# Optimization experiments

Hardware: AMD Instinct MI355X
Metric: run time of the kernel (lower is better)

Reference implementation:

```python
import jax, jax.numpy as jnp
import numpy as np

EMB_DIM = 1024
HEAD_DIM = 128
BLOCK_SIZE = 2048
BATCH = 8


def setup_inputs() -> dict:
    key = jax.random.key(0)
    kx, kq, kk, kv = jax.random.split(key, 4)
    x = jax.random.normal(kx, (BATCH, BLOCK_SIZE, EMB_DIM), dtype=jnp.float32)
    # nn.Linear(emb_dim, head_dim, bias=False) weights have shape [head_dim, emb_dim]
    s = 1.0 / np.sqrt(EMB_DIM)
    Wq = jax.random.uniform(kq, (HEAD_DIM, EMB_DIM), jnp.float32, -s, s)
    Wk = jax.random.uniform(kk, (HEAD_DIM, EMB_DIM), jnp.float32, -s, s)
    Wv = jax.random.uniform(kv, (HEAD_DIM, EMB_DIM), jnp.float32, -s, s)
    return {"x": x, "Wq": Wq, "Wk": Wk, "Wv": Wv}


def reference(x, Wq, Wk, Wv):
    # x: [b, t, c]; W*: [h, c]  (torch Linear applies x @ W.T)
    b, t, c = x.shape
    h = Wq.shape[0]
    q = jnp.einsum("btc,hc->bth", x, Wq)
    k = jnp.einsum("btc,hc->bth", x, Wk)
    v = jnp.einsum("btc,hc->bth", x, Wv)
    scores = jnp.einsum("bth,bsh->bts", q, k) * (h ** -0.5)  # [b, t, t]
    causal = jnp.tril(jnp.ones((t, t), dtype=bool))
    scores = jnp.where(causal, scores, -jnp.inf)
    attn = jax.nn.softmax(scores, axis=-1)
    # dropout is identity in eval / deterministic mode
    return jnp.einsum("bts,bsh->bth", attn, v)
```

## Files before the change

### kernel.cpp

```cpp
#include <hip/hip_runtime.h>
#include <hip/hip_bf16.h>

#define TT 2048
#define CC 1024
#define DD 128
#define BB 8
#define BK 32
#define NSTEP (CC / BK)

typedef __attribute__((ext_vector_type(8))) short bf16x8;
typedef __attribute__((ext_vector_type(4))) float f32x4;
typedef __attribute__((ext_vector_type(16))) float f32x16;
typedef __attribute__((ext_vector_type(4))) short short4v;

__device__ inline short f2bf(float f) {
    union { float f; unsigned u; } v; v.f = f;
    unsigned r = v.u + 0x7FFFu + ((v.u >> 16) & 1u);
    return (short)(r >> 16);
}

__device__ inline unsigned pack2(float lo, float hi) {
    return (unsigned)(unsigned short)f2bf(lo) | ((unsigned)(unsigned short)f2bf(hi) << 16);
}

#define GLOAD16(gp, lp) __builtin_amdgcn_global_load_lds(                       \
    (const __attribute__((address_space(1))) unsigned int*)(const void*)(gp),   \
    (__attribute__((address_space(3))) unsigned int*)(void*)(lp), 16, 0, 0)

__global__ __launch_bounds__(256) void prep_w(const float* __restrict__ Wq,
                                              const float* __restrict__ Wk,
                                              const float* __restrict__ Wv,
                                              short* __restrict__ Wall) {
    int row = blockIdx.x;
    const float* src = row < 128 ? Wq + (size_t)row * CC
                     : row < 256 ? Wk + (size_t)(row - 128) * CC
                                 : Wv + (size_t)(row - 256) * CC;
    short* dst = Wall + (size_t)row * CC;
    int j = threadIdx.x * 4;
    float4 f = *(const float4*)(src + j);
    short4v s = { f2bf(f.x), f2bf(f.y), f2bf(f.z), f2bf(f.w) };
    *(short4v*)(dst + j) = s;
}

__global__ __launch_bounds__(256) void qkv_fused(const float* __restrict__ X,
                                                 const short* __restrict__ Wall,
                                                 short* __restrict__ Q,
                                                 short* __restrict__ K,
                                                 short* __restrict__ Vs) {
    __shared__ char lds[2 * 16384];
    int tid = threadIdx.x, lane = tid & 63, wid = tid >> 6;
    int wm = wid >> 1, wn = wid & 1;
    int lg = lane >> 4, lr = lane & 15;
    int m0 = blockIdx.x * 64;
    int n0 = blockIdx.y * 128;

    int rA = tid >> 3;
    int cA = (tid & 7) * 16;
    int sA = cA ^ ((rA & 7) << 4);
    const char* gA0 = (const char*)(X + (size_t)(m0 + rA) * CC) + sA;
    const char* gA1 = (const char*)(X + (size_t)(m0 + rA + 32) * CC) + sA;
    int rB = tid >> 2, cB = (tid & 3) * 16;
    const char* gB0 = (const char*)(Wall + (size_t)(n0 + rB) * CC) + cB;
    const char* gB1 = (const char*)(Wall + (size_t)(n0 + rB + 64) * CC) + cB;

    f32x4 acc[2][4] = {};

#define STAGEF(t_, buf_) do {                                                   \
        char* b_ = lds + (buf_) * 16384;                                        \
        size_t ka_ = (size_t)(t_) * 128;             \
        size_t kb_ = (size_t)(t_) * 64;              \
        GLOAD16(gA0 + ka_, b_ + tid * 16);                                      \
        GLOAD16(gA1 + ka_, b_ + 4096 + tid * 16);                               \
        GLOAD16(gB0 + kb_, b_ + 8192 + tid * 16);                               \
        GLOAD16(gB1 + kb_, b_ + 12288 + tid * 16);                              \
    } while (0)

#define KSTEPF(buf_) do {                                                       \
        const char* b_ = lds + (buf_) * 16384;                                  \
        bf16x8 a_[2], bb_[4];                                                   \
        int swz_ = (lr & 7) << 4;                                               \
        _Pragma("unroll")                                                       \
        for (int mi = 0; mi < 2; ++mi) {                                        \
            const char* Ap_ = b_ + (wm * 32 + mi * 16 + lr) * 128;              \
            f32x4 lo_ = *(const f32x4*)(Ap_ + ((lg * 32) ^ swz_));              \
            f32x4 hi_ = *(const f32x4*)(Ap_ + ((lg * 32 + 16) ^ swz_));         \
            bf16x8 t_;                                                          \
            t_[0] = f2bf(lo_[0]); t_[1] = f2bf(lo_[1]);                         \
            t_[2] = f2bf(lo_[2]); t_[3] = f2bf(lo_[3]);                         \
            t_[4] = f2bf(hi_[0]); t_[5] = f2bf(hi_[1]);                         \
            t_[6] = f2bf(hi_[2]); t_[7] = f2bf(hi_[3]);                         \
            a_[mi] = t_;                                                        \
        }                                                                       \
        _Pragma("unroll")                                                       \
        for (int nj = 0; nj < 4; ++nj)                                          \
            bb_[nj] = *(const bf16x8*)(b_ + 8192 + (wn*64 + nj*16 + lr) * 64 + lg*16);\
        _Pragma("unroll")                                                       \
        for (int mi = 0; mi < 2; ++mi)                                          \
            _Pragma("unroll")                                                   \
            for (int nj = 0; nj < 4; ++nj)                                      \
                acc[mi][nj] = __builtin_amdgcn_mfma_f32_16x16x32_bf16(a_[mi], bb_[nj], acc[mi][nj], 0, 0, 0);\
    } while (0)

    STAGEF(0, 0);
#pragma unroll 2
    for (int t = 0; t < NSTEP; ++t) {
        __syncthreads();
        if (t + 1 < NSTEP) STAGEF(t + 1, (t + 1) & 1);
        KSTEPF(t & 1);
    }
#undef STAGEF
#undef KSTEPF

    int bidx = m0 >> 11;
    int nt = blockIdx.y;
#pragma unroll
    for (int mi = 0; mi < 2; ++mi) {
        int row = m0 + wm * 32 + mi * 16 + lg * 4;
        int t = row - bidx * TT;
#pragma unroll
        for (int nj = 0; nj < 4; ++nj) {
            int col = wn * 64 + nj * 16 + lr;
            if (nt == 0) {
                short* dst = Q + ((size_t)bidx * TT + t) * DD + col;
#pragma unroll
                for (int r = 0; r < 4; ++r) dst[(size_t)r * DD] = f2bf(acc[mi][nj][r]);
            } else if (nt == 1) {
                short* dst = K + ((size_t)bidx * TT + t) * DD + col;
#pragma unroll
                for (int r = 0; r < 4; ++r) dst[(size_t)r * DD] = f2bf(acc[mi][nj][r]);
            } else {
                short4v v4;
#pragma unroll
                for (int r = 0; r < 4; ++r) v4[r] = f2bf(acc[mi][nj][r]);
                *(short4v*)(Vs + (size_t)bidx * TT * DD
                               + (size_t)(t >> 4) * 2048 + col * 16 + (t & 15)) = v4;
            }
        }
    }
}

#define PV_CHUNK(WS, H, CB) do {                                                   \
    unsigned a0 = WS[4*(H)+0], a1 = WS[4*(H)+1];                                   \
    unsigned b0 = WS[4*(H)+2], b1 = WS[4*(H)+3];                                   \
    unsigned xa0 = (unsigned)__shfl_xor((int)a0, 32, 64);                          \
    unsigned xa1 = (unsigned)__shfl_xor((int)a1, 32, 64);                          \
    unsigned xb0 = (unsigned)__shfl_xor((int)b0, 32, 64);                          \
    unsigned xb1 = (unsigned)__shfl_xor((int)b1, 32, 64);                          \
    union { unsigned u[4]; bf16x8 v; } pu;                                         \
    pu.u[0] = lg2 ? xb0 : a0;                                                      \
    pu.u[1] = lg2 ? xb1 : a1;                                                      \
    pu.u[2] = lg2 ? b0  : xa0;                                                     \
    pu.u[3] = lg2 ? b1  : xa1;                                                     \
    const short* Vp = Vb + ((size_t)((kbase >> 4) + (CB)) * 128 + q) * 16 + lg2 * 8;\
    _Pragma("unroll")                                                              \
    for (int dt = 0; dt < 4; ++dt) {                                               \
        bf16x8 vf = *(const bf16x8*)(Vp + dt * 512);                               \
        acc[dt] = __builtin_amdgcn_mfma_f32_32x32x16_bf16(vf, pu.v, acc[dt], 0,0,0);\
    }                                                                              \
} while (0)

__global__ __launch_bounds__(256) void attn32(const short* __restrict__ Q,
                                              const short* __restrict__ K,
                                              const short* __restrict__ Vt,
                                              float* __restrict__ out) {
    __shared__ float slot[2][4][32][33];
    __shared__ float ml[2][2][32];

    int tid = threadIdx.x;
    int lane = tid & 63, w = tid >> 6;
    int q = lane & 31, lg2 = lane >> 5;
    int bid = blockIdx.x;
    int b = bid & 7;
    int qt = 63 - (bid >> 3);
    int r0 = qt * 32;
    int qq = r0 + q;

    const short* Qb = Q + (size_t)b * TT * DD;
    const short* Kb = K + (size_t)b * TT * DD;
    const short* Vb = Vt + (size_t)b * TT * DD;

    bf16x8 qf[8];
#pragma unroll
    for (int kc = 0; kc < 8; ++kc)
        qf[kc] = *(const bf16x8*)(Qb + (size_t)qq * DD + kc * 16 + lg2 * 8);

    f32x16 acc[4] = {};
    float mb = -INFINITY, l = 0.f;
    const float scale = 0.08838834764831845f;
    int kend = r0 + 32;

    for (int kt = w; kt * 64 < kend; kt += 4) {
        int kbase = kt * 64;
        f32x16 s0 = {}, s1 = {};
        const short* Kp0 = Kb + (size_t)(kbase + q) * DD + lg2 * 8;
        const short* Kp1 = Kp0 + (size_t)32 * DD;
        __builtin_amdgcn_s_setprio(1);
#pragma unroll
        for (int kc = 0; kc < 8; ++kc) {
            bf16x8 k0 = *(const bf16x8*)(Kp0 + kc * 16);
            bf16x8 k1 = *(const bf16x8*)(Kp1 + kc * 16);
            s0 = __builtin_amdgcn_mfma_f32_32x32x16_bf16(k0, qf[kc], s0, 0, 0, 0);
            s1 = __builtin_amdgcn_mfma_f32_32x32x16_bf16(k1, qf[kc], s1, 0, 0, 0);
        }
        __builtin_amdgcn_s_setprio(0);

        if (kbase + 63 > r0) {
#pragma unroll
            for (int r = 0; r < 16; ++r) {
                int kl = (r & 3) + 8 * (r >> 2) + 4 * lg2;
                s0[r] = (kbase + kl > qq) ? -INFINITY : s0[r] * scale;
                s1[r] = (kbase + 32 + kl > qq) ? -INFINITY : s1[r] * scale;
            }
        } else {
#pragma unroll
            for (int r = 0; r < 16; ++r) { s0[r] *= scale; s1[r] *= scale; }
        }

        float tmx[16];
#pragma unroll
        for (int r = 0; r < 16; ++r) tmx[r] = fmaxf(s0[r], s1[r]);
#pragma unroll
        for (int st = 8; st; st >>= 1)
#pragma unroll
            for (int r = 0; r < 8; ++r) if (r < st) tmx[r] = fmaxf(tmx[r], tmx[r + st]);
        float pm = fmaxf(tmx[0], __shfl_xor(tmx[0], 32, 64));

        if (__any(pm > mb + 8.f)) {
            float mn = fmaxf(mb, pm);
            float mc = (mn == -INFINITY) ? 0.f : mn;
            float sc = __expf(mb - mc);
            mb = mc; l *= sc;
#pragma unroll
            for (int dt = 0; dt < 4; ++dt)
#pragma unroll
                for (int r = 0; r < 16; ++r) acc[dt][r] *= sc;
        }

#pragma unroll
        for (int r = 0; r < 16; ++r) { s0[r] = __expf(s0[r] - mb); s1[r] = __expf(s1[r] - mb); }

        float ts[16];
#pragma unroll
        for (int r = 0; r < 16; ++r) ts[r] = s0[r] + s1[r];
#pragma unroll
        for (int st = 8; st; st >>= 1)
#pragma unroll
            for (int r = 0; r < 8; ++r) if (r < st) ts[r] += ts[r + st];
        l += ts[0] + __shfl_xor(ts[0], 32, 64);

        unsigned w0[8], w1[8];
#pragma unroll
        for (int k2 = 0; k2 < 8; ++k2) {
            w0[k2] = pack2(s0[2 * k2], s0[2 * k2 + 1]);
            w1[k2] = pack2(s1[2 * k2], s1[2 * k2 + 1]);
        }

        __builtin_amdgcn_s_setprio(1);
        PV_CHUNK(w0, 0, 0);
        PV_CHUNK(w0, 1, 1);
        PV_CHUNK(w1, 0, 2);
        PV_CHUNK(w1, 1, 3);
        __builtin_amdgcn_s_setprio(0);
    }

    if (w >= 2) {
        int s = w - 2;
#pragma unroll
        for (int dt = 0; dt < 4; ++dt)
#pragma unroll
            for (int r = 0; r < 16; ++r)
                slot[s][dt][(r & 3) + 8 * (r >> 2) + 4 * lg2][q] = acc[dt][r];
        if (lg2 == 0) { ml[s][0][q] = mb; ml[s][1][q] = l; }
    }
    __syncthreads();
    if (w < 2) {
        int s = w;
        float m2 = ml[s][0][q], l2 = ml[s][1][q];
        float M = fmaxf(mb, m2);
        float Mc = (M == -INFINITY) ? 0.f : M;
        float e1 = __expf(mb - Mc), e2 = __expf(m2 - Mc);
        mb = Mc; l = l * e1 + l2 * e2;
#pragma unroll
        for (int dt = 0; dt < 4; ++dt)
#pragma unroll
            for (int r = 0; r < 16; ++r)
                acc[dt][r] = acc[dt][r] * e1 + slot[s][dt][(r & 3) + 8 * (r >> 2) + 4 * lg2][q] * e2;
    }
    __syncthreads();
    if (w == 1) {
#pragma unroll
        for (int dt = 0; dt < 4; ++dt)
#pragma unroll
            for (int r = 0; r < 16; ++r)
                slot[0][dt][(r & 3) + 8 * (r >> 2) + 4 * lg2][q] = acc[dt][r];
        if (lg2 == 0) { ml[0][0][q] = mb; ml[0][1][q] = l; }
    }
    __syncthreads();
    if (w == 0) {
        float m2 = ml[0][0][q], l2 = ml[0][1][q];
        float M = fmaxf(mb, m2);
        float Mc = (M == -INFINITY) ? 0.f : M;
        float e1 = __expf(mb - Mc), e2 = __expf(m2 - Mc);
        l = l * e1 + l2 * e2;
        float inv = 1.f / l;
#pragma unroll
        for (int dt = 0; dt < 4; ++dt)
#pragma unroll
            for (int rq = 0; rq < 4; ++rq) {
                f32x4 o4;
#pragma unroll
                for (int j = 0; j < 4; ++j) {
                    int r = rq * 4 + j;
                    o4[j] = (acc[dt][r] * e1 + slot[0][dt][(r & 3) + 8 * rq + 4 * lg2][q] * e2) * inv;
                }
                *(f32x4*)(out + ((size_t)b * TT + qq) * DD + dt * 32 + rq * 8 + lg2 * 4) = o4;
            }
    }
}

extern "C" void kernel_launch(void* const* d_in, const int* in_sizes, int n_in,
                              void* d_out, int out_size, void* d_ws, size_t ws_size,
                              hipStream_t stream) {
    const float* x  = (const float*)d_in[0];
    const float* Wq = (const float*)d_in[1];
    const float* Wk = (const float*)d_in[2];
    const float* Wv = (const float*)d_in[3];
    float* out = (float*)d_out;

    char* ws = (char*)d_ws;
    short* Wall = (short*)ws;
    short* Q    = (short*)(ws + 786432);
    short* K    = (short*)(ws + 786432 + 4194304);
    short* Vs   = (short*)(ws + 786432 + 2 * 4194304);

    prep_w<<<384, 256, 0, stream>>>(Wq, Wk, Wv, Wall);
    qkv_fused<<<dim3(256, 3), 256, 0, stream>>>(x, Wall, Q, K, Vs);
    attn32<<<BB * 64, 256, 0, stream>>>(Q, K, Vs, out);
}
```

Baseline: 83.80 us.

## Compute QKV in one pass per row tile and prefetch V fragments early

The QKV projection kernel now uses 512-thread blocks that each compute all 384 output columns for a 64-row tile. Each fp32 X tile is loaded once instead of three times across separate grid columns, which cuts X traffic and repeated bf16 conversion, but the grid drops to 256 blocks and LDS and register use grow. In the attention kernel, all V fragments for a key tile are loaded right after the QK MFMAs so their latency overlaps the softmax, and the s_setprio hints are removed. The V prefetch adds 64 VGPRs per thread, which may reduce occupancy.

```diff
diff --git a/kernel.cpp b/kernel.cpp
--- a/kernel.cpp
+++ b/kernel.cpp
@@ -42,42 +42,37 @@
     *(short4v*)(dst + j) = s;
 }
 
-__global__ __launch_bounds__(256) void qkv_fused(const float* __restrict__ X,
-                                                 const short* __restrict__ Wall,
-                                                 short* __restrict__ Q,
-                                                 short* __restrict__ K,
-                                                 short* __restrict__ Vs) {
-    __shared__ char lds[2 * 16384];
+__global__ __launch_bounds__(512) void qkv_onepass(const float* __restrict__ X,
+                                                   const short* __restrict__ Wall,
+                                                   short* __restrict__ Q,
+                                                   short* __restrict__ K,
+                                                   short* __restrict__ Vs) {
+    __shared__ char lds[2 * 32768];
     int tid = threadIdx.x, lane = tid & 63, wid = tid >> 6;
-    int wm = wid >> 1, wn = wid & 1;
+    int wm = wid >> 2, wn = wid & 3;
     int lg = lane >> 4, lr = lane & 15;
     int m0 = blockIdx.x * 64;
-    int n0 = blockIdx.y * 128;
-
-    int rA = tid >> 3;
-    int cA = (tid & 7) * 16;
+
+    int rA = tid >> 3, cA = (tid & 7) * 16;
     int sA = cA ^ ((rA & 7) << 4);
-    const char* gA0 = (const char*)(X + (size_t)(m0 + rA) * CC) + sA;
-    const char* gA1 = (const char*)(X + (size_t)(m0 + rA + 32) * CC) + sA;
-    int rB = tid >> 2, cB = (tid & 3) * 16;
-    const char* gB0 = (const char*)(Wall + (size_t)(n0 + rB) * CC) + cB;
-    const char* gB1 = (const char*)(Wall + (size_t)(n0 + rB + 64) * CC) + cB;
-
-    f32x4 acc[2][4] = {};
-
-#define STAGEF(t_, buf_) do {                                                   \
-        char* b_ = lds + (buf_) * 16384;                                        \
-        size_t ka_ = (size_t)(t_) * 128;             \
-        size_t kb_ = (size_t)(t_) * 64;              \
-        GLOAD16(gA0 + ka_, b_ + tid * 16);                                      \
-        GLOAD16(gA1 + ka_, b_ + 4096 + tid * 16);                               \
-        GLOAD16(gB0 + kb_, b_ + 8192 + tid * 16);                               \
-        GLOAD16(gB1 + kb_, b_ + 12288 + tid * 16);                              \
+    const char* gA = (const char*)(X + (size_t)(m0 + rA) * CC) + sA;
+    int rB0 = tid >> 2, cB = (tid & 3) * 16;
+    const char* gB = (const char*)Wall + cB;
+
+    f32x4 acc[2][6] = {};
+
+#define STAGE1(t_, buf_) do {                                                   \
+        char* b_ = lds + (buf_) * 32768;                                        \
+        GLOAD16(gA + (size_t)(t_) * 128, b_ + tid * 16);                        \
+        _Pragma("unroll")                                                       \
+        for (int i_ = 0; i_ < 3; ++i_)                                          \
+            GLOAD16(gB + (size_t)(rB0 + i_ * 128) * 2048 + (size_t)(t_) * 64,   \
+                    b_ + 8192 + (tid + i_ * 512) * 16);                         \
     } while (0)
 
-#define KSTEPF(buf_) do {                                                       \
-        const char* b_ = lds + (buf_) * 16384;                                  \
-        bf16x8 a_[2], bb_[4];                                                   \
+#define KSTEP1(buf_) do {                                                       \
+        const char* b_ = lds + (buf_) * 32768;                                  \
+        bf16x8 a_[2], bb_[6];                                                   \
         int swz_ = (lr & 7) << 4;                                               \
         _Pragma("unroll")                                                       \
         for (int mi = 0; mi < 2; ++mi) {                                        \
@@ -92,40 +87,39 @@
             a_[mi] = t_;                                                        \
         }                                                                       \
         _Pragma("unroll")                                                       \
-        for (int nj = 0; nj < 4; ++nj)                                          \
-            bb_[nj] = *(const bf16x8*)(b_ + 8192 + (wn*64 + nj*16 + lr) * 64 + lg*16);\
+        for (int nj = 0; nj < 6; ++nj)                                          \
+            bb_[nj] = *(const bf16x8*)(b_ + 8192 + (wn*96 + nj*16 + lr) * 64 + lg*16);\
         _Pragma("unroll")                                                       \
         for (int mi = 0; mi < 2; ++mi)                                          \
             _Pragma("unroll")                                                   \
-            for (int nj = 0; nj < 4; ++nj)                                      \
+            for (int nj = 0; nj < 6; ++nj)                                      \
                 acc[mi][nj] = __builtin_amdgcn_mfma_f32_16x16x32_bf16(a_[mi], bb_[nj], acc[mi][nj], 0, 0, 0);\
     } while (0)
 
-    STAGEF(0, 0);
+    STAGE1(0, 0);
 #pragma unroll 2
     for (int t = 0; t < NSTEP; ++t) {
         __syncthreads();
-        if (t + 1 < NSTEP) STAGEF(t + 1, (t + 1) & 1);
-        KSTEPF(t & 1);
-    }
-#undef STAGEF
-#undef KSTEPF
+        if (t + 1 < NSTEP) STAGE1(t + 1, (t + 1) & 1);
+        KSTEP1(t & 1);
+    }
+#undef STAGE1
+#undef KSTEP1
 
     int bidx = m0 >> 11;
-    int nt = blockIdx.y;
 #pragma unroll
     for (int mi = 0; mi < 2; ++mi) {
         int row = m0 + wm * 32 + mi * 16 + lg * 4;
         int t = row - bidx * TT;
 #pragma unroll
-        for (int nj = 0; nj < 4; ++nj) {
-            int col = wn * 64 + nj * 16 + lr;
-            if (nt == 0) {
+        for (int nj = 0; nj < 6; ++nj) {
+            int col = wn * 96 + nj * 16 + lr;
+            if (col < 128) {
                 short* dst = Q + ((size_t)bidx * TT + t) * DD + col;
 #pragma unroll
                 for (int r = 0; r < 4; ++r) dst[(size_t)r * DD] = f2bf(acc[mi][nj][r]);
-            } else if (nt == 1) {
-                short* dst = K + ((size_t)bidx * TT + t) * DD + col;
+            } else if (col < 256) {
+                short* dst = K + ((size_t)bidx * TT + t) * DD + (col - 128);
 #pragma unroll
                 for (int r = 0; r < 4; ++r) dst[(size_t)r * DD] = f2bf(acc[mi][nj][r]);
             } else {
@@ -133,7 +127,7 @@
 #pragma unroll
                 for (int r = 0; r < 4; ++r) v4[r] = f2bf(acc[mi][nj][r]);
                 *(short4v*)(Vs + (size_t)bidx * TT * DD
-                               + (size_t)(t >> 4) * 2048 + col * 16 + (t & 15)) = v4;
+                               + (size_t)(t >> 4) * 2048 + (col - 256) * 16 + (t & 15)) = v4;
             }
         }
     }
@@ -151,12 +145,9 @@
     pu.u[1] = lg2 ? xb1 : a1;                                                      \
     pu.u[2] = lg2 ? b0  : xa0;                                                     \
     pu.u[3] = lg2 ? b1  : xa1;                                                     \
-    const short* Vp = Vb + ((size_t)((kbase >> 4) + (CB)) * 128 + q) * 16 + lg2 * 8;\
     _Pragma("unroll")                                                              \
-    for (int dt = 0; dt < 4; ++dt) {                                               \
-        bf16x8 vf = *(const bf16x8*)(Vp + dt * 512);                               \
-        acc[dt] = __builtin_amdgcn_mfma_f32_32x32x16_bf16(vf, pu.v, acc[dt], 0,0,0);\
-    }                                                                              \
+    for (int dt = 0; dt < 4; ++dt)                                                 \
+        acc[dt] = __builtin_amdgcn_mfma_f32_32x32x16_bf16(vf[CB][dt], pu.v, acc[dt], 0,0,0);\
 } while (0)
 
 __global__ __launch_bounds__(256) void attn32(const short* __restrict__ Q,
@@ -194,7 +185,6 @@
         f32x16 s0 = {}, s1 = {};
         const short* Kp0 = Kb + (size_t)(kbase + q) * DD + lg2 * 8;
         const short* Kp1 = Kp0 + (size_t)32 * DD;
-        __builtin_amdgcn_s_setprio(1);
 #pragma unroll
         for (int kc = 0; kc < 8; ++kc) {
             bf16x8 k0 = *(const bf16x8*)(Kp0 + kc * 16);
@@ -202,7 +192,15 @@
             s0 = __builtin_amdgcn_mfma_f32_32x32x16_bf16(k0, qf[kc], s0, 0, 0, 0);
             s1 = __builtin_amdgcn_mfma_f32_32x32x16_bf16(k1, qf[kc], s1, 0, 0, 0);
         }
-        __builtin_amdgcn_s_setprio(0);
+
+        bf16x8 vf[4][4];
+#pragma unroll
+        for (int cb = 0; cb < 4; ++cb) {
+            const short* Vp = Vb + ((size_t)((kbase >> 4) + cb) * 128 + q) * 16 + lg2 * 8;
+#pragma unroll
+            for (int dt = 0; dt < 4; ++dt)
+                vf[cb][dt] = *(const bf16x8*)(Vp + dt * 512);
+        }
 
         if (kbase + 63 > r0) {
 #pragma unroll
@@ -255,12 +253,10 @@
             w1[k2] = pack2(s1[2 * k2], s1[2 * k2 + 1]);
         }
 
-        __builtin_amdgcn_s_setprio(1);
         PV_CHUNK(w0, 0, 0);
         PV_CHUNK(w0, 1, 1);
         PV_CHUNK(w1, 0, 2);
         PV_CHUNK(w1, 1, 3);
-        __builtin_amdgcn_s_setprio(0);
     }
 
     if (w >= 2) {
@@ -334,6 +330,6 @@
     short* Vs   = (short*)(ws + 786432 + 2 * 4194304);
 
     prep_w<<<384, 256, 0, stream>>>(Wq, Wk, Wv, Wall);
-    qkv_fused<<<dim3(256, 3), 256, 0, stream>>>(x, Wall, Q, K, Vs);
+    qkv_onepass<<<256, 512, 0, stream>>>(x, Wall, Q, K, Vs);
     attn32<<<BB * 64, 256, 0, stream>>>(Q, K, Vs, out);
 }
```

Measured after the change: 71.26 us. -15.0%, faster.
